# Optimization experiments

Hardware: AMD Instinct MI355X
Metric: run time of the kernel (lower is better)

## Reference

```python
import jax, jax.numpy as jnp
import numpy as np

B, T, D, H = 2, 2048, 1024, 16
HD = D // H  # 64
EPS = 1e-5

def _ln(x, g, b):
    mu = jnp.mean(x, axis=-1, keepdims=True)
    var = jnp.mean(jnp.square(x - mu), axis=-1, keepdims=True)
    return (x - mu) * jax.lax.rsqrt(var + EPS) * g + b

def setup_inputs() -> dict:
    key = jax.random.key(0)
    ks = jax.random.split(key, 12)
    s = 0.02
    return {
        "x":  jax.random.normal(ks[0], (B, T, D), jnp.float32),
        "Wq": jax.random.normal(ks[1], (H, D, HD), jnp.float32) * s,
        "Wk": jax.random.normal(ks[2], (H, D, HD), jnp.float32) * s,
        "Wv": jax.random.normal(ks[3], (H, D, HD), jnp.float32) * s,
        "Wo": jax.random.normal(ks[4], (D, D), jnp.float32) * s,
        "bo": jnp.zeros((D,), jnp.float32),
        "W1": jax.random.normal(ks[5], (D, 4 * D), jnp.float32) * s,
        "b1": jnp.zeros((4 * D,), jnp.float32),
        "W2": jax.random.normal(ks[6], (4 * D, D), jnp.float32) * s,
        "b2": jnp.zeros((D,), jnp.float32),
        "ln1_g": jnp.ones((D,), jnp.float32),
        "ln1_b": jnp.zeros((D,), jnp.float32),
        "ln2_g": jnp.ones((D,), jnp.float32),
        "ln2_b": jnp.zeros((D,), jnp.float32),
    }

def reference(x, Wq, Wk, Wv, Wo, bo, W1, b1, W2, b2, ln1_g, ln1_b, ln2_g, ln2_b):
    b, t, d = x.shape
    # --- self-attention on ln1(x) ---
    h = _ln(x, ln1_g, ln1_b)
    q = jnp.einsum('btd,hde->bhte', h, Wq)  # [B,H,T,hd]
    k = jnp.einsum('btd,hde->bhte', h, Wk)
    v = jnp.einsum('btd,hde->bhte', h, Wv)
    # NOTE: original code scales by C**-0.5 with C = N_EMBED (not head_size)
    wei = jnp.einsum('bhte,bhse->bhts', q, k) * (d ** -0.5)
    causal = jnp.tril(jnp.ones((t, t), bool))
    wei = jnp.where(causal, wei, -jnp.inf)
    att = jax.nn.softmax(wei, axis=-1)
    o = jnp.einsum('bhts,bhse->bhte', att, v)
    o = o.transpose(0, 2, 1, 3).reshape(b, t, d)  # concat heads
    x = x + o @ Wo + bo
    # --- feed-forward on ln2(x) ---
    h2 = _ln(x, ln2_g, ln2_b)
    ff = jax.nn.relu(h2 @ W1 + b1) @ W2 + b2
    return x + ff
```

## Files before the change

### kernel.cpp

```cpp
#include <hip/hip_runtime.h>
#include <stdint.h>

typedef unsigned short u16;
typedef __attribute__((ext_vector_type(8))) short bf16x8;
typedef __attribute__((ext_vector_type(4))) float f32x4;
typedef __attribute__((ext_vector_type(4))) unsigned int u32x4;
typedef __attribute__((ext_vector_type(2))) unsigned int u32x2;
typedef __attribute__((ext_vector_type(4))) unsigned short u16x4;

#define MFMA16(a, b, c) __builtin_amdgcn_mfma_f32_16x16x32_bf16(a, b, c, 0, 0, 0)
#define VMCNT(N) asm volatile("s_waitcnt vmcnt(" #N ")" ::: "memory")
#define LGKM0() asm volatile("s_waitcnt lgkmcnt(0)" ::: "memory")

__device__ __forceinline__ u16 f2bf(float f) {
  union { float f; uint32_t u; } v; v.f = f;
  uint32_t r = v.u + 0x7FFFu + ((v.u >> 16) & 1u);
  return (u16)(r >> 16);
}

__device__ __forceinline__ float bf2f(u16 u) {
  union { uint32_t u; float f; } v; v.u = ((uint32_t)u) << 16;
  return v.f;
}

__device__ __forceinline__ uint32_t cvt_pk_bf16(float a, float b) {
  uint32_t r;
  asm("v_cvt_pk_bf16_f32 %0, %1, %2" : "=v"(r) : "v"(a), "v"(b));
  return r;
}

__device__ __forceinline__ void gload_lds16(const u16* g, u16* l) {
  __builtin_amdgcn_global_load_lds((const __attribute__((address_space(1))) void*)(g),
                                   (__attribute__((address_space(3))) void*)(l), 16, 0, 0);
}

__global__ __launch_bounds__(256) void prep_kernel(
    const float* __restrict__ x, const float* __restrict__ g1,
    const float* __restrict__ be1, u16* __restrict__ h,
    const float* __restrict__ Wq, const float* __restrict__ Wk,
    const float* __restrict__ Wv, u16* __restrict__ BtQKV,
    const float* __restrict__ Wo, u16* __restrict__ WoT,
    const float* __restrict__ W1, u16* __restrict__ W1T,
    const float* __restrict__ W2, u16* __restrict__ W2T) {
  __shared__ float tile[32][33];
  __shared__ float red[8];
  int bid = blockIdx.x, tid = threadIdx.x;
  if (bid < 4096) {
    int row = bid;
    float4 v = ((const float4*)(x + (size_t)row * 1024))[tid];
    float s = v.x + v.y + v.z + v.w;
    float ss = v.x * v.x + v.y * v.y + v.z * v.z + v.w * v.w;
#pragma unroll
    for (int m = 1; m < 64; m <<= 1) { s += __shfl_xor(s, m); ss += __shfl_xor(ss, m); }
    int wave = tid >> 6, lane = tid & 63;
    if (lane == 0) { red[wave] = s; red[4 + wave] = ss; }
    __syncthreads();
    s = red[0] + red[1] + red[2] + red[3];
    ss = red[4] + red[5] + red[6] + red[7];
    float mean = s * (1.0f / 1024.0f);
    float var = ss * (1.0f / 1024.0f) - mean * mean;
    float rstd = rsqrtf(var + 1e-5f);
    float4 gv = ((const float4*)g1)[tid];
    float4 bv = ((const float4*)be1)[tid];
    u16x4 o;
    o.x = f2bf((v.x - mean) * rstd * gv.x + bv.x);
    o.y = f2bf((v.y - mean) * rstd * gv.y + bv.y);
    o.z = f2bf((v.z - mean) * rstd * gv.z + bv.z);
    o.w = f2bf((v.w - mean) * rstd * gv.w + bv.w);
    *(u16x4*)(h + (size_t)row * 1024 + tid * 4) = o;
    return;
  }
  const float* I;
  u16* O;
  int K, N, n0, k0;
  if (bid < 7168) {
    int idx = bid - 4096;
    int bz = idx >> 6, by = (idx >> 1) & 31, bx = idx & 1;
    int ww = bz >> 4, head = bz & 15;
    I = ((ww == 0) ? Wq : (ww == 1) ? Wk : Wv) + (size_t)head * 65536;
    O = BtQKV + (size_t)ww * 1048576 + (size_t)head * 65536;
    K = 1024; N = 64; n0 = bx * 32; k0 = by * 32;
  } else if (bid < 8192) {
    int idx = bid - 7168;
    I = Wo; O = WoT; K = 1024; N = 1024;
    n0 = (idx & 31) * 32; k0 = (idx >> 5) * 32;
  } else if (bid < 12288) {
    int idx = bid - 8192;
    I = W1; O = W1T; K = 1024; N = 4096;
    n0 = (idx & 127) * 32; k0 = (idx >> 7) * 32;
  } else {
    int idx = bid - 12288;
    I = W2; O = W2T; K = 4096; N = 1024;
    n0 = (idx & 31) * 32; k0 = (idx >> 5) * 32;
  }
  int tx = tid & 31, ty = tid >> 5;
#pragma unroll
  for (int i = 0; i < 4; i++)
    tile[ty + i * 8][tx] = I[(size_t)(k0 + ty + i * 8) * N + n0 + tx];
  __syncthreads();
#pragma unroll
  for (int i = 0; i < 4; i++)
    O[(size_t)(n0 + ty + i * 8) * K + k0 + tx] = f2bf(tile[tx][ty + i * 8]);
}

__global__ __launch_bounds__(256) void ln_kernel(const float* __restrict__ x,
                                                 const float* __restrict__ g,
                                                 const float* __restrict__ beta,
                                                 u16* __restrict__ out) {
  int row = blockIdx.x;
  int tid = threadIdx.x;
  float4 v = ((const float4*)(x + (size_t)row * 1024))[tid];
  float s = v.x + v.y + v.z + v.w;
  float ss = v.x * v.x + v.y * v.y + v.z * v.z + v.w * v.w;
#pragma unroll
  for (int m = 1; m < 64; m <<= 1) { s += __shfl_xor(s, m); ss += __shfl_xor(ss, m); }
  __shared__ float red[8];
  int wave = tid >> 6, lane = tid & 63;
  if (lane == 0) { red[wave] = s; red[4 + wave] = ss; }
  __syncthreads();
  s = red[0] + red[1] + red[2] + red[3];
  ss = red[4] + red[5] + red[6] + red[7];
  float mean = s * (1.0f / 1024.0f);
  float var = ss * (1.0f / 1024.0f) - mean * mean;
  float rstd = rsqrtf(var + 1e-5f);
  float4 gv = ((const float4*)g)[tid];
  float4 bv = ((const float4*)beta)[tid];
  u16x4 o;
  o.x = f2bf((v.x - mean) * rstd * gv.x + bv.x);
  o.y = f2bf((v.y - mean) * rstd * gv.y + bv.y);
  o.z = f2bf((v.z - mean) * rstd * gv.z + bv.z);
  o.w = f2bf((v.w - mean) * rstd * gv.w + bv.w);
  *(u16x4*)(out + (size_t)row * 1024 + tid * 4) = o;
}

template <int EP>
__global__ __launch_bounds__(512, 2) void gemm8p(const u16* __restrict__ A,
                                                 const u16* __restrict__ Bt,
                                                 int M, int N, int K, int KS,
                                                 void* __restrict__ out0,
                                                 u16* __restrict__ out1,
                                                 u16* __restrict__ out2,
                                                 const float* __restrict__ bias) {
  __shared__ __align__(16) u16 lds[65536];
  const int tid = threadIdx.x;
  const int lane = tid & 63, wave = tid >> 6;
  const int lo = lane & 15, hi = lane >> 4;
  const int wm = wave >> 2, wn = wave & 3;
  int gx = gridDim.x;
  int lin = blockIdx.y * gx + blockIdx.x;
  int nwg = gx * gridDim.y;
  int cpx = nwg >> 3;
  int swz = (lin & 7) * cpx + (lin >> 3);
  int bm0 = (swz / gx) * 256, bn0 = (swz % gx) * 256;
  int kbeg = blockIdx.z * KS;
  int T = KS >> 6;

  int rs_ = tid >> 3, ss_ = (tid & 7) ^ (rs_ & 7);
  const u16* srcA = A + (size_t)(bm0 + rs_) * K + kbeg + ss_ * 8;
  const u16* srcB = Bt + (size_t)(bn0 + rs_) * K + kbeg + ss_ * 8;
  const size_t i1 = (size_t)64 * K;
  const size_t h1 = (size_t)128 * K;
  const int dst0 = wave * 512;
  const int dst1 = 4096 + wave * 512;

  const int rpA = wm * 16 + lo;
  const int rpB = wn * 16 + lo;
  const int sp0 = (hi ^ (lo & 7)) * 8;

  f32x4 acc[8][4] = {};
  bf16x8 a[4][2], b0[2][2], b1[2][2];

  auto stageA = [&](int buf, int h, int koff) {
    const u16* s = srcA + koff + (h ? h1 : 0);
    u16* d = lds + (buf * 2 + h) * 8192;
    gload_lds16(s, d + dst0);
    gload_lds16(s + i1, d + dst1);
  };
  auto stageB = [&](int buf, int h, int koff) {
    const u16* s = srcB + koff + (h ? h1 : 0);
    u16* d = lds + 32768 + (buf * 2 + h) * 8192;
    gload_lds16(s, d + dst0);
    gload_lds16(s + i1, d + dst1);
  };
  auto loadA = [&](int buf, int h) {
    const u16* base = lds + (buf * 2 + h) * 8192 + rpA * 64;
#pragma unroll
    for (int m = 0; m < 4; m++) {
      a[m][0] = *(const bf16x8*)(base + m * 2048 + sp0);
      a[m][1] = *(const bf16x8*)(base + m * 2048 + (sp0 ^ 32));
    }
  };
  auto loadB = [&](bf16x8 (&bb)[2][2], int buf, int g) {
    const u16* base = lds + 32768 + (buf * 2 + g) * 8192 + rpB * 64;
#pragma unroll
    for (int n = 0; n < 2; n++) {
      bb[n][0] = *(const bf16x8*)(base + n * 4096 + sp0);
      bb[n][1] = *(const bf16x8*)(base + n * 4096 + (sp0 ^ 32));
    }
  };
  auto mmac = [&](int mh, int np, bf16x8 (&bb)[2][2]) {
    __builtin_amdgcn_s_setprio(1);
#pragma unroll
    for (int m = 0; m < 4; m++)
#pragma unroll
      for (int n = 0; n < 2; n++) {
        acc[mh + m][np + n] = MFMA16(a[m][0], bb[n][0], acc[mh + m][np + n]);
        acc[mh + m][np + n] = MFMA16(a[m][1], bb[n][1], acc[mh + m][np + n]);
      }
    __builtin_amdgcn_s_setprio(0);
  };

  stageA(0, 0, 0); stageB(0, 0, 0); stageB(0, 1, 0); stageA(0, 1, 0);
  VMCNT(4);
  __builtin_amdgcn_s_barrier();

  for (int t = 0; t < T; ++t) {
    int cur = t & 1, nxt = cur ^ 1;
    bool more = (t + 1 < T);
    int koff = (t + 1) * 64;
    loadA(cur, 0); loadB(b0, cur, 0);
    if (more) stageA(nxt, 0, koff);
    __builtin_amdgcn_s_barrier();
    LGKM0();
    __builtin_amdgcn_sched_barrier(0);
    mmac(0, 0, b0);
    __builtin_amdgcn_s_barrier();
    loadB(b1, cur, 1);
    if (more) { stageB(nxt, 0, koff); VMCNT(6); } else { VMCNT(2); }
    __builtin_amdgcn_s_barrier();
    LGKM0();
    __builtin_amdgcn_sched_barrier(0);
    mmac(0, 2, b1);
    __builtin_amdgcn_s_barrier();
    loadA(cur, 1);
    if (more) { stageB(nxt, 1, koff); VMCNT(6); } else { VMCNT(0); }
    __builtin_amdgcn_s_barrier();
    LGKM0();
    __builtin_amdgcn_sched_barrier(0);
    mmac(4, 0, b0);
    __builtin_amdgcn_s_barrier();
    if (more) { stageA(nxt, 1, koff); VMCNT(4); }
    __builtin_amdgcn_s_barrier();
    mmac(4, 2, b1);
    __builtin_amdgcn_s_barrier();
  }

  const int sec = (EP == 0) ? (bn0 >> 10) : 0;
#pragma unroll
  for (int mt = 0; mt < 8; mt++) {
    int gr0 = bm0 + (mt >> 2) * 128 + (mt & 3) * 32 + wm * 16 + hi * 4;
#pragma unroll
    for (int nt = 0; nt < 4; nt++) {
      int gc = bn0 + (nt >> 1) * 128 + (nt & 1) * 64 + wn * 16 + lo;
      if constexpr (EP == 0) {
        int b_ = gr0 >> 11, t_ = gr0 & 2047;
        int nn = gc & 1023, h_ = nn >> 6, e_ = nn & 63;
        size_t bh = (size_t)(b_ * 16 + h_);
        if (sec == 2) {
          u32x2 w;
          w.x = cvt_pk_bf16(acc[mt][nt][0], acc[mt][nt][1]);
          w.y = cvt_pk_bf16(acc[mt][nt][2], acc[mt][nt][3]);
          *(u32x2*)(out2 + (bh * 64 + e_) * 2048 + t_) = w;
        } else {
          float sc = (sec == 0) ? 0.0450842200f : 1.0f;
          u16* dst = (sec == 0) ? (u16*)out0 : out1;
#pragma unroll
          for (int j = 0; j < 4; j++)
            dst[(bh * 2048 + t_ + j) * 64 + e_] = f2bf(acc[mt][nt][j] * sc);
        }
      } else if constexpr (EP == 2) {
#pragma unroll
        for (int j = 0; j < 4; j++) {
          int gr = gr0 + j;
          float v = acc[mt][nt][j] + bias[gc];
          ((u16*)out0)[(size_t)gr * N + gc] = f2bf(fmaxf(v, 0.0f));
        }
      }
    }
  }
}

__global__ __launch_bounds__(256, 2) void gemm128(const u16* __restrict__ A,
                                                  const u16* __restrict__ Bt,
                                                  int M, int N, int K,
                                                  const float* __restrict__ bias,
                                                  const float* __restrict__ res,
                                                  float* __restrict__ out) {
  __shared__ __align__(16) u16 lds[32768];
  const int tid = threadIdx.x;
  const int lane = tid & 63, wave = tid >> 6;
  const int lo = lane & 15, hi = lane >> 4;
  const int wm = wave >> 1, wn = wave & 1;
  int gx = gridDim.x;
  int lin = blockIdx.y * gx + blockIdx.x;
  int nwg = gx * gridDim.y;
  int cpx = nwg >> 3;
  int swz = (lin & 7) * cpx + (lin >> 3);
  int bm0 = (swz / gx) * 128, bn0 = (swz % gx) * 128;
  int T = K >> 6;

  int rs_ = tid >> 3, ss_ = (tid & 7) ^ (rs_ & 7);
  const u16* srcA = A + (size_t)(bm0 + rs_) * K + ss_ * 8;
  const u16* srcB = Bt + (size_t)(bn0 + rs_) * K + ss_ * 8;
  const size_t i1 = (size_t)32 * K;
  const size_t h1 = (size_t)64 * K;
  const int dst0 = wave * 512;
  const int dst1 = 2048 + wave * 512;

  const int sp0 = (hi ^ (lo & 7)) * 8;

  f32x4 acc[4][4] = {};
  bf16x8 a[4][2], b[4][2];

  auto stageA = [&](int buf, int h, int koff) {
    const u16* s = srcA + koff + (h ? h1 : 0);
    u16* d = lds + (buf * 2 + h) * 4096;
    gload_lds16(s, d + dst0);
    gload_lds16(s + i1, d + dst1);
  };
  auto stageB = [&](int buf, int h, int koff) {
    const u16* s = srcB + koff + (h ? h1 : 0);
    u16* d = lds + 16384 + (buf * 2 + h) * 4096;
    gload_lds16(s, d + dst0);
    gload_lds16(s + i1, d + dst1);
  };
  auto loadAh = [&](int buf, int h) {
    const u16* base = lds + (buf * 2 + h) * 4096;
#pragma unroll
    for (int m = 0; m < 2; m++) {
      int lr = m * 32 + wm * 16 + lo;
      a[h * 2 + m][0] = *(const bf16x8*)(base + lr * 64 + sp0);
      a[h * 2 + m][1] = *(const bf16x8*)(base + lr * 64 + (sp0 ^ 32));
    }
  };
  auto loadBh = [&](int buf, int h) {
    const u16* base = lds + 16384 + (buf * 2 + h) * 4096;
#pragma unroll
    for (int n = 0; n < 2; n++) {
      int lr = n * 32 + wn * 16 + lo;
      b[h * 2 + n][0] = *(const bf16x8*)(base + lr * 64 + sp0);
      b[h * 2 + n][1] = *(const bf16x8*)(base + lr * 64 + (sp0 ^ 32));
    }
  };
  auto mmac = [&](int mb, int nb) {
    __builtin_amdgcn_s_setprio(1);
#pragma unroll
    for (int m = 0; m < 2; m++)
#pragma unroll
      for (int n = 0; n < 2; n++) {
        acc[mb + m][nb + n] = MFMA16(a[mb + m][0], b[nb + n][0], acc[mb + m][nb + n]);
        acc[mb + m][nb + n] = MFMA16(a[mb + m][1], b[nb + n][1], acc[mb + m][nb + n]);
      }
    __builtin_amdgcn_s_setprio(0);
  };

  stageA(0, 0, 0); stageB(0, 0, 0); stageB(0, 1, 0); stageA(0, 1, 0);
  VMCNT(4);
  __builtin_amdgcn_s_barrier();

  for (int t = 0; t < T; ++t) {
    int cur = t & 1, nxt = cur ^ 1;
    bool more = (t + 1 < T);
    int koff = (t + 1) * 64;
    loadAh(cur, 0); loadBh(cur, 0);
    if (more) { stageA(nxt, 0, koff); VMCNT(4); } else { VMCNT(2); }
    __builtin_amdgcn_s_barrier();
    LGKM0();
    __builtin_amdgcn_sched_barrier(0);
    mmac(0, 0);
    __builtin_amdgcn_s_barrier();
    loadBh(cur, 1);
    if (more) { stageB(nxt, 0, koff); VMCNT(4); } else { VMCNT(0); }
    __builtin_amdgcn_s_barrier();
    LGKM0();
    __builtin_amdgcn_sched_barrier(0);
    mmac(0, 2);
    __builtin_amdgcn_s_barrier();
    loadAh(cur, 1);
    if (more) stageB(nxt, 1, koff);
    __builtin_amdgcn_s_barrier();
    LGKM0();
    __builtin_amdgcn_sched_barrier(0);
    mmac(2, 0);
    __builtin_amdgcn_s_barrier();
    if (more) { stageA(nxt, 1, koff); VMCNT(4); }
    __builtin_amdgcn_s_barrier();
    mmac(2, 2);
    __builtin_amdgcn_s_barrier();
  }

#pragma unroll
  for (int mt = 0; mt < 4; mt++) {
    int gr0 = bm0 + mt * 32 + wm * 16 + hi * 4;
#pragma unroll
    for (int nt = 0; nt < 4; nt++) {
      int gc = bn0 + nt * 32 + wn * 16 + lo;
      float bb = bias[gc];
#pragma unroll
      for (int j = 0; j < 4; j++) {
        int gr = gr0 + j;
        out[(size_t)gr * N + gc] = acc[mt][nt][j] + bb + res[(size_t)gr * N + gc];
      }
    }
  }
}

__global__ __launch_bounds__(512, 4) void attn_kernel(const u16* __restrict__ q,
                                                      const u16* __restrict__ k,
                                                      const u16* __restrict__ vt,
                                                      u16* __restrict__ o) {
  __shared__ __align__(16) u16 Ks[2][64 * 64];
  __shared__ __align__(16) u16 Vs[2][64 * 64];
  __shared__ __align__(16) u16 Ps[8][16 * 72];
  int bh = blockIdx.y;
  int pi = blockIdx.x;
  int tid = threadIdx.x, lane = tid & 63, wave = tid >> 6;
  int lo = lane & 15, hi = lane >> 4;
  int grp = wave >> 2;
  int qblk_w = grp ? pi : (31 - pi);
  int qb0 = qblk_w * 64;
  int nkb = 32 - pi;
  const u16* qbase = q + (size_t)bh * 2048 * 64;
  const u16* kbase = k + (size_t)bh * 2048 * 64;
  const u16* vbase = vt + (size_t)bh * 64 * 2048;

  int srow = tid >> 3;
  int ssl = (tid & 7) ^ (srow & 7);
  int kOff = srow * 64 + ssl * 8;
  int vOff = srow * 2048 + ssl * 8;

  int qrow = qb0 + (wave & 3) * 16 + lo;
  bf16x8 qf0 = *(const bf16x8*)(qbase + (size_t)qrow * 64 + hi * 8);
  bf16x8 qf1 = *(const bf16x8*)(qbase + (size_t)qrow * 64 + 32 + hi * 8);

  float l_r = 0.0f;
  f32x4 of[4] = {};
  u16* Pw = Ps[wave];

  auto stage = [&](int b, int kb) {
    gload_lds16(kbase + (size_t)kb * 4096 + kOff, Ks[b] + wave * 512);
    gload_lds16(vbase + kb * 64 + vOff, Vs[b] + wave * 512);
  };

  stage(0, 0);
  __syncthreads();

  for (int kb = 0; kb < nkb; kb++) {
    int cur = kb & 1;
    if (kb + 1 < nkb) stage(cur ^ 1, kb + 1);
    if (kb <= qblk_w) {
      const u16* Kb = Ks[cur];
      const u16* Vb = Vs[cur];
      f32x4 s4[4] = {};
#pragma unroll
      for (int nt = 0; nt < 4; nt++) {
        int r = nt * 16 + lo, rw = r & 7;
        bf16x8 kf0 = *(const bf16x8*)(Kb + r * 64 + ((hi ^ rw) << 3));
        bf16x8 kf1 = *(const bf16x8*)(Kb + r * 64 + (((hi + 4) ^ rw) << 3));
        s4[nt] = MFMA16(kf0, qf0, s4[nt]);
        s4[nt] = MFMA16(kf1, qf1, s4[nt]);
      }
      float rs = 0.0f;
      bool diag = (kb == qblk_w);
#pragma unroll
      for (int nt = 0; nt < 4; nt++) {
        float e0, e1, e2, e3;
        if (diag) {
          int key = kb * 64 + nt * 16 + hi * 4;
          e0 = (key     > qrow) ? 0.0f : __builtin_amdgcn_exp2f(s4[nt][0]);
          e1 = (key + 1 > qrow) ? 0.0f : __builtin_amdgcn_exp2f(s4[nt][1]);
          e2 = (key + 2 > qrow) ? 0.0f : __builtin_amdgcn_exp2f(s4[nt][2]);
          e3 = (key + 3 > qrow) ? 0.0f : __builtin_amdgcn_exp2f(s4[nt][3]);
        } else {
          e0 = __builtin_amdgcn_exp2f(s4[nt][0]);
          e1 = __builtin_amdgcn_exp2f(s4[nt][1]);
          e2 = __builtin_amdgcn_exp2f(s4[nt][2]);
          e3 = __builtin_amdgcn_exp2f(s4[nt][3]);
        }
        rs += (e0 + e1) + (e2 + e3);
        u32x2 w;
        w.x = cvt_pk_bf16(e0, e1);
        w.y = cvt_pk_bf16(e2, e3);
        *(u32x2*)(Pw + lo * 72 + nt * 16 + hi * 4) = w;
      }
      rs += __shfl_xor(rs, 16);
      rs += __shfl_xor(rs, 32);
      l_r += rs;
      bf16x8 pb0 = *(const bf16x8*)(Pw + lo * 72 + hi * 8);
      bf16x8 pb1 = *(const bf16x8*)(Pw + lo * 72 + 32 + hi * 8);
#pragma unroll
      for (int et = 0; et < 4; et++) {
        int e = et * 16 + lo, ew = e & 7;
        bf16x8 v0 = *(const bf16x8*)(Vb + e * 64 + ((hi ^ ew) << 3));
        bf16x8 v1 = *(const bf16x8*)(Vb + e * 64 + (((hi + 4) ^ ew) << 3));
        of[et] = MFMA16(v0, pb0, of[et]);
        of[et] = MFMA16(v1, pb1, of[et]);
      }
    }
    __syncthreads();
  }
  int hh = bh & 15, bb = bh >> 4;
  float inv = 1.0f / l_r;
  size_t obase = ((size_t)(bb * 2048 + qrow)) * 1024 + hh * 64 + hi * 4;
#pragma unroll
  for (int et = 0; et < 4; et++) {
    u32x2 w;
    w.x = cvt_pk_bf16(of[et][0] * inv, of[et][1] * inv);
    w.y = cvt_pk_bf16(of[et][2] * inv, of[et][3] * inv);
    *(u32x2*)(o + obase + et * 16) = w;
  }
}

extern "C" void kernel_launch(void* const* d_in, const int* in_sizes, int n_in,
                              void* d_out, int out_size, void* d_ws, size_t ws_size,
                              hipStream_t stream) {
  const float* x = (const float*)d_in[0];
  const float* Wq = (const float*)d_in[1];
  const float* Wk = (const float*)d_in[2];
  const float* Wv = (const float*)d_in[3];
  const float* Wo = (const float*)d_in[4];
  const float* bo = (const float*)d_in[5];
  const float* W1 = (const float*)d_in[6];
  const float* b1 = (const float*)d_in[7];
  const float* W2 = (const float*)d_in[8];
  const float* b2 = (const float*)d_in[9];
  const float* g1 = (const float*)d_in[10];
  const float* be1 = (const float*)d_in[11];
  const float* g2 = (const float*)d_in[12];
  const float* be2 = (const float*)d_in[13];
  float* out = (float*)d_out;
  char* ws = (char*)d_ws;
  const size_t MB = 1024ull * 1024ull;

  u16* h = (u16*)(ws + 0);
  u16* o = h;
  u16* BtQKV = (u16*)(ws + 8 * MB);
  u16* WoT = (u16*)(ws + 14 * MB);
  u16* W1T = (u16*)(ws + 16 * MB);
  u16* W2T = (u16*)(ws + 64 * MB);
  u16* qb = (u16*)(ws + 32 * MB);
  u16* kb = (u16*)(ws + 40 * MB);
  u16* vtb = (u16*)(ws + 48 * MB);
  u16* h2 = (u16*)(ws + 8 * MB);
  u16* yb = (u16*)(ws + 32 * MB);

  prep_kernel<<<16384, 256, 0, stream>>>(x, g1, be1, h, Wq, Wk, Wv, BtQKV,
                                         Wo, WoT, W1, W1T, W2, W2T);
  gemm8p<0><<<dim3(12, 16), 512, 0, stream>>>(h, BtQKV, 4096, 3072, 1024, 1024,
                                              (void*)qb, kb, vtb, nullptr);
  attn_kernel<<<dim3(16, 32), 512, 0, stream>>>(qb, kb, vtb, o);
  gemm128<<<dim3(8, 32), 256, 0, stream>>>(o, WoT, 4096, 1024, 1024, bo, x, out);
  ln_kernel<<<4096, 256, 0, stream>>>(out, g2, be2, h2);
  gemm8p<2><<<dim3(16, 16), 512, 0, stream>>>(h2, W1T, 4096, 4096, 1024, 1024,
                                              (void*)yb, nullptr, nullptr, b1);
  gemm128<<<dim3(8, 32), 256, 0, stream>>>(yb, W2T, 4096, 1024, 4096, b2, out, out);
}
```

Baseline: 207.8 us.

## Restructure gemm128 to 512 threads with 128-wide K tiles

New measurement: 197.6 us. 4.9% less time.

```diff
diff --git a/kernel.cpp b/kernel.cpp
--- a/kernel.cpp
+++ b/kernel.cpp
@@ -280,13 +280,13 @@
   }
 }
 
-__global__ __launch_bounds__(256, 2) void gemm128(const u16* __restrict__ A,
+__global__ __launch_bounds__(512, 2) void gemm128(const u16* __restrict__ A,
                                                   const u16* __restrict__ Bt,
                                                   int M, int N, int K,
                                                   const float* __restrict__ bias,
                                                   const float* __restrict__ res,
                                                   float* __restrict__ out) {
-  __shared__ __align__(16) u16 lds[32768];
+  __shared__ __align__(16) u16 lds[65536];
   const int tid = threadIdx.x;
   const int lane = tid & 63, wave = tid >> 6;
   const int lo = lane & 15, hi = lane >> 4;
@@ -297,60 +297,55 @@
   int cpx = nwg >> 3;
   int swz = (lin & 7) * cpx + (lin >> 3);
   int bm0 = (swz / gx) * 128, bn0 = (swz % gx) * 128;
-  int T = K >> 6;
-
-  int rs_ = tid >> 3, ss_ = (tid & 7) ^ (rs_ & 7);
+  int T = K >> 7;
+
+  int rs_ = tid >> 4, ss_ = (tid & 15) ^ (rs_ & 15);
   const u16* srcA = A + (size_t)(bm0 + rs_) * K + ss_ * 8;
   const u16* srcB = Bt + (size_t)(bn0 + rs_) * K + ss_ * 8;
   const size_t i1 = (size_t)32 * K;
   const size_t h1 = (size_t)64 * K;
   const int dst0 = wave * 512;
-  const int dst1 = 2048 + wave * 512;
-
-  const int sp0 = (hi ^ (lo & 7)) * 8;
-
-  f32x4 acc[4][4] = {};
-  bf16x8 a[4][2], b[4][2];
+  const int dst1 = 4096 + wave * 512;
+
+  const int rA = wm * 16 + lo;
+  const int cB = wn * 16 + lo;
+
+  f32x4 acc[2][4] = {};
+  bf16x8 a[4], b0[2][4], b1[2][4];
 
   auto stageA = [&](int buf, int h, int koff) {
     const u16* s = srcA + koff + (h ? h1 : 0);
-    u16* d = lds + (buf * 2 + h) * 4096;
+    u16* d = lds + (buf * 2 + h) * 8192;
     gload_lds16(s, d + dst0);
     gload_lds16(s + i1, d + dst1);
   };
   auto stageB = [&](int buf, int h, int koff) {
     const u16* s = srcB + koff + (h ? h1 : 0);
-    u16* d = lds + 16384 + (buf * 2 + h) * 4096;
+    u16* d = lds + 32768 + (buf * 2 + h) * 8192;
     gload_lds16(s, d + dst0);
     gload_lds16(s + i1, d + dst1);
   };
-  auto loadAh = [&](int buf, int h) {
-    const u16* base = lds + (buf * 2 + h) * 4096;
-#pragma unroll
-    for (int m = 0; m < 2; m++) {
-      int lr = m * 32 + wm * 16 + lo;
-      a[h * 2 + m][0] = *(const bf16x8*)(base + lr * 64 + sp0);
-      a[h * 2 + m][1] = *(const bf16x8*)(base + lr * 64 + (sp0 ^ 32));
-    }
-  };
-  auto loadBh = [&](int buf, int h) {
-    const u16* base = lds + 16384 + (buf * 2 + h) * 4096;
-#pragma unroll
-    for (int n = 0; n < 2; n++) {
-      int lr = n * 32 + wn * 16 + lo;
-      b[h * 2 + n][0] = *(const bf16x8*)(base + lr * 64 + sp0);
-      b[h * 2 + n][1] = *(const bf16x8*)(base + lr * 64 + (sp0 ^ 32));
-    }
-  };
-  auto mmac = [&](int mb, int nb) {
+  auto loadA_ = [&](int buf, int h) {
+    const u16* base = lds + (buf * 2 + h) * 8192 + rA * 128;
+#pragma unroll
+    for (int kk = 0; kk < 4; kk++)
+      a[kk] = *(const bf16x8*)(base + (((kk * 4 + hi) ^ lo) << 3));
+  };
+  auto loadB_ = [&](bf16x8 (&bb)[2][4], int buf, int g) {
+    const u16* base = lds + 32768 + (buf * 2 + g) * 8192 + cB * 128;
+#pragma unroll
+    for (int n = 0; n < 2; n++)
+#pragma unroll
+      for (int kk = 0; kk < 4; kk++)
+        bb[n][kk] = *(const bf16x8*)(base + n * 4096 + (((kk * 4 + hi) ^ lo) << 3));
+  };
+  auto mmac = [&](int mt, int g, bf16x8 (&bb)[2][4]) {
     __builtin_amdgcn_s_setprio(1);
 #pragma unroll
-    for (int m = 0; m < 2; m++)
-#pragma unroll
-      for (int n = 0; n < 2; n++) {
-        acc[mb + m][nb + n] = MFMA16(a[mb + m][0], b[nb + n][0], acc[mb + m][nb + n]);
-        acc[mb + m][nb + n] = MFMA16(a[mb + m][1], b[nb + n][1], acc[mb + m][nb + n]);
-      }
+    for (int n = 0; n < 2; n++)
+#pragma unroll
+      for (int kk = 0; kk < 4; kk++)
+        acc[mt][g * 2 + n] = MFMA16(a[kk], bb[n][kk], acc[mt][g * 2 + n]);
     __builtin_amdgcn_s_setprio(0);
   };
 
@@ -361,37 +356,37 @@
   for (int t = 0; t < T; ++t) {
     int cur = t & 1, nxt = cur ^ 1;
     bool more = (t + 1 < T);
-    int koff = (t + 1) * 64;
-    loadAh(cur, 0); loadBh(cur, 0);
-    if (more) { stageA(nxt, 0, koff); VMCNT(4); } else { VMCNT(2); }
+    int koff = (t + 1) * 128;
+    loadA_(cur, 0); loadB_(b0, cur, 0);
+    if (more) stageA(nxt, 0, koff);
     __builtin_amdgcn_s_barrier();
     LGKM0();
     __builtin_amdgcn_sched_barrier(0);
-    mmac(0, 0);
-    __builtin_amdgcn_s_barrier();
-    loadBh(cur, 1);
-    if (more) { stageB(nxt, 0, koff); VMCNT(4); } else { VMCNT(0); }
+    mmac(0, 0, b0);
+    __builtin_amdgcn_s_barrier();
+    loadB_(b1, cur, 1);
+    if (more) { stageB(nxt, 0, koff); VMCNT(6); } else { VMCNT(2); }
     __builtin_amdgcn_s_barrier();
     LGKM0();
     __builtin_amdgcn_sched_barrier(0);
-    mmac(0, 2);
-    __builtin_amdgcn_s_barrier();
-    loadAh(cur, 1);
-    if (more) stageB(nxt, 1, koff);
+    mmac(0, 1, b1);
+    __builtin_amdgcn_s_barrier();
+    loadA_(cur, 1);
+    if (more) { stageB(nxt, 1, koff); VMCNT(6); } else { VMCNT(0); }
     __builtin_amdgcn_s_barrier();
     LGKM0();
     __builtin_amdgcn_sched_barrier(0);
-    mmac(2, 0);
+    mmac(1, 0, b0);
     __builtin_amdgcn_s_barrier();
     if (more) { stageA(nxt, 1, koff); VMCNT(4); }
     __builtin_amdgcn_s_barrier();
-    mmac(2, 2);
-    __builtin_amdgcn_s_barrier();
-  }
-
-#pragma unroll
-  for (int mt = 0; mt < 4; mt++) {
-    int gr0 = bm0 + mt * 32 + wm * 16 + hi * 4;
+    mmac(1, 1, b1);
+    __builtin_amdgcn_s_barrier();
+  }
+
+#pragma unroll
+  for (int mt = 0; mt < 2; mt++) {
+    int gr0 = bm0 + mt * 64 + wm * 16 + hi * 4;
 #pragma unroll
     for (int nt = 0; nt < 4; nt++) {
       int gc = bn0 + nt * 32 + wn * 16 + lo;
@@ -549,9 +544,9 @@
   gemm8p<0><<<dim3(12, 16), 512, 0, stream>>>(h, BtQKV, 4096, 3072, 1024, 1024,
                                               (void*)qb, kb, vtb, nullptr);
   attn_kernel<<<dim3(16, 32), 512, 0, stream>>>(qb, kb, vtb, o);
-  gemm128<<<dim3(8, 32), 256, 0, stream>>>(o, WoT, 4096, 1024, 1024, bo, x, out);
+  gemm128<<<dim3(8, 32), 512, 0, stream>>>(o, WoT, 4096, 1024, 1024, bo, x, out);
   ln_kernel<<<4096, 256, 0, stream>>>(out, g2, be2, h2);
   gemm8p<2><<<dim3(16, 16), 512, 0, stream>>>(h2, W1T, 4096, 4096, 1024, 1024,
                                               (void*)yb, nullptr, nullptr, b1);
-  gemm128<<<dim3(8, 32), 256, 0, stream>>>(yb, W2T, 4096, 1024, 4096, b2, out, out);
-}
+  gemm128<<<dim3(8, 32), 512, 0, stream>>>(yb, W2T, 4096, 1024, 4096, b2, out, out);
+}
```
